# Optimization experiments

Hardware: AMD Instinct MI355X
Metric: run time of the kernel (lower is better)

## Reference

```python
import jax, jax.numpy as jnp
import numpy as np
from jax import lax

B, C, H, Wd = 8, 3, 256, 256
K = 32           # kernels
LAT = K * 8      # 256, latent dim
P = 7            # patch size
HALF = P // 2
S = 1024         # samples per image
PD = C * P * P   # 147
NEG = 0.01       # LeakyReLU slope
EPS = 1e-5


def setup_inputs() -> dict:
    key = jax.random.key(0)
    ks = jax.random.split(key, 20)
    x = jax.random.normal(ks[0], (B, C, H, Wd), dtype=jnp.float32)
    # patch centers must satisfy HALF <= c <= H-1-HALF (here [3, 252])
    anchors_hw = jax.random.randint(ks[1], (B, S, 2), HALF, H - HALF, dtype=jnp.int32)
    positives_hw = jax.random.randint(ks[2], (B, S, 2), HALF, H - HALF, dtype=jnp.int32)
    def w(k, shape, fan_in):
        return jax.random.normal(k, shape, dtype=jnp.float32) * (1.0 / np.sqrt(fan_in))
    inp = dict(x=x, anchors_hw=anchors_hw, positives_hw=positives_hw,
               w1=w(ks[3], (K, C, 3, 3), C * 9),        g1=jnp.ones((K,), jnp.float32),        b1=jnp.zeros((K,), jnp.float32),
               w2=w(ks[4], (2 * K, K, 3, 3), K * 9),    g2=jnp.ones((2 * K,), jnp.float32),    b2=jnp.zeros((2 * K,), jnp.float32),
               w3=w(ks[5], (4 * K, 2 * K, 3, 3), 2 * K * 9), g3=jnp.ones((4 * K,), jnp.float32), b3=jnp.zeros((4 * K,), jnp.float32),
               w4=w(ks[6], (8 * K, 4 * K, 3, 3), 4 * K * 9), g4=jnp.ones((8 * K,), jnp.float32), b4=jnp.zeros((8 * K,), jnp.float32),
               lin1_w=w(ks[7], (PD, LAT), LAT), lin1_b=jnp.zeros((PD,), jnp.float32),
               lin2_w=w(ks[8], (PD, PD), PD),   lin2_b=jnp.zeros((PD,), jnp.float32))
    return inp


def _conv(x, w):
    return lax.conv_general_dilated(x, w, (1, 1), 'SAME',
                                    dimension_numbers=('NCHW', 'OIHW', 'NCHW'))


def _bn(x, g, b):
    # training-mode BatchNorm2d: batch stats over (N,H,W)
    m = x.mean(axis=(0, 2, 3), keepdims=True)
    v = x.var(axis=(0, 2, 3), keepdims=True)
    return g[None, :, None, None] * (x - m) * lax.rsqrt(v + EPS) + b[None, :, None, None]


def _lrelu(x):
    return jnp.where(x >= 0, x, NEG * x)


def _forward(x, anchors_hw, positives_hw, w1, g1, b1, w2, g2, b2, w3, g3, b3,
             w4, g4, b4, lin1_w, lin1_b, lin2_w, lin2_b):
    feat = _lrelu(_bn(_conv(x, w1), g1, b1))
    feat = _lrelu(_bn(_conv(feat, w2), g2, b2))
    feat = _lrelu(_bn(_conv(feat, w3), g3, b3))
    feat = _lrelu(_bn(_conv(feat, w4), g4, b4))  # [B, LAT, H, W]

    fhwc = jnp.transpose(feat, (0, 2, 3, 1))  # [B,H,W,LAT]
    gather_pts = jax.vmap(lambda f, hw: f[hw[:, 0], hw[:, 1]])  # per-batch fancy gather
    W_anchors = gather_pts(fhwc, anchors_hw)      # [B,S,LAT]
    W_positives = gather_pts(fhwc, positives_hw)  # [B,S,LAT]

    def slice_one(img, hw):  # img [C,H,W], hw [2]
        return lax.dynamic_slice(img, (0, hw[0] - HALF, hw[1] - HALF), (C, P, P))
    patch_real = jax.vmap(jax.vmap(slice_one, in_axes=(None, 0)))(x, anchors_hw)  # [B,S,C,P,P]

    h = _lrelu(jnp.einsum('bsl,pl->bsp', W_anchors, lin1_w) + lin1_b)
    patch_recon = (jnp.einsum('bsp,qp->bsq', h, lin2_w) + lin2_b).reshape(x.shape[0], -1, C, P, P)
    return (feat, patch_real, patch_recon, W_anchors, W_positives)


def reference(x, anchors_hw, positives_hw, w1, g1, b1, w2, g2, b2, w3, g3, b3,
              w4, g4, b4, lin1_w, lin1_b, lin2_w, lin2_b):
    return _forward(x, anchors_hw, positives_hw, w1, g1, b1, w2, g2, b2,
                    w3, g3, b3, w4, g4, b4, lin1_w, lin1_b, lin2_w, lin2_b)
```

## Files before the change

kernel.cpp:

```cpp
#include <hip/hip_runtime.h>
#include <hip/hip_bf16.h>

typedef unsigned short u16;
typedef short bf16x8 __attribute__((ext_vector_type(8)));
typedef float f32x4 __attribute__((ext_vector_type(4)));
typedef unsigned short u16x8 __attribute__((ext_vector_type(8)));

#define PD 147

static const long OFF_PREAL = 134217728L;
static const long OFF_PRECON= 135421952L;
static const long OFF_WA    = 136626176L;
static const long OFF_WP    = 138723328L;

static const long RAW_SPLIT = 100663296L;

__device__ __forceinline__ float lrelu(float v){ return v >= 0.f ? v : 0.01f*v; }

__device__ __forceinline__ float bf2f(u16 u){
    union { unsigned int i; float f; } x; x.i = ((unsigned int)u) << 16; return x.f;
}
__device__ __forceinline__ u16 f2bf(float f){
    __hip_bfloat16 h = __float2bfloat16(f);
    return *reinterpret_cast<u16*>(&h);
}

__device__ __forceinline__ void gload16(const void* g, void* l){
    __builtin_amdgcn_global_load_lds((const __attribute__((address_space(1))) void*)g,
                                     (__attribute__((address_space(3))) void*)l, 16, 0, 0);
}

template<int CIN, int KOUT, bool SPLIT>
__global__ __launch_bounds__(512)
void conv_mfma(const u16* __restrict__ fin, const u16* __restrict__ wt,
               const float* __restrict__ ssin,
               void* __restrict__ out_, u16* __restrict__ rawhi,
               float* __restrict__ part)
{
    constexpr int CC = CIN / 32;
    constexpr int NS3 = CC * 3;
    constexpr int NF = KOUT / 64;
    constexpr int ABYTES = 2 * 324 * 32 * 2;
    constexpr int BQ = 3 * KOUT * 4;
    constexpr int NB3 = (BQ + 511) / 512;
    constexpr int BBYTES = 2 * BQ * 16;
    constexpr int EPIB = 256 * KOUT * 2;
    constexpr int SB = (ABYTES + BBYTES) > EPIB ? (ABYTES + BBYTES) : EPIB;
    __shared__ __align__(16) char smem[SB];
    u16* As = (u16*)smem;
    u16* Bs = (u16*)(smem + ABYTES);

    const int tid = threadIdx.x;
    const int w = tid >> 6, lane = tid & 63;
    const int wm = w >> 2, wn = w & 3;
    const int tile = blockIdx.x;
    const int tx0 = (tile & 15) << 4, ty0 = (tile >> 4) << 4;
    const int b = blockIdx.y;
    const long pixbase = (long)b << 16;
    const int hi = lane >> 4;
    const int quarter = lane & 3;

    f32x4 acc[8][NF];
#pragma unroll
    for (int m = 0; m < 8; m++)
#pragma unroll
        for (int n = 0; n < NF; n++) acc[m][n] = (f32x4){0.f,0.f,0.f,0.f};

    float sc8[8], sh8[8];
    auto load_ss = [&](int cc){
        int c0 = cc*32 + quarter*8;
#pragma unroll
        for (int j = 0; j < 8; j++){
            sc8[j] = ssin[c0 + j];
            sh8[j] = ssin[CIN + c0 + j];
        }
    };

    auto stage_a_round = [&](int cc, int buf, int r){
        int q = r*512 + w*64 + lane;
        int pf = q >> 2;
        int ly = pf / 18, lx = pf - ly*18;
        int gy = ty0 + ly - 1, gx = tx0 + lx - 1;
        bool ok = (q < 1296) && ((unsigned)gy < 256u) && ((unsigned)gx < 256u);
        u16x8 o = (u16x8){0,0,0,0,0,0,0,0};
        if (ok){
            u16x8 v = *(const u16x8*)(fin + ((pixbase + (gy<<8) + gx) * CIN + cc*32 + quarter*8));
#pragma unroll
            for (int j = 0; j < 8; j++)
                o[j] = f2bf(lrelu(sc8[j]*bf2f(v[j]) + sh8[j]));
        }
        if (q < 1296)
            *(u16x8*)(As + buf*(324*32) + q*8) = o;
    };
    auto stage_b3 = [&](int s, int buf){
        int cc = s / 3, dyr = s - cc*3;
        int t0 = dyr * 3;
        u16* dstbase = Bs + buf * (BQ*16/2);
#pragma unroll
        for (int r = 0; r < NB3; ++r){
            int q = r*512 + w*64 + lane;
            int tl = q / (KOUT*4);
            int qq = q - tl*(KOUT*4);
            int k = qq >> 2, bq = qq & 3;
            const u16* src = wt + (((long)(t0+tl)*KOUT + k) * CIN + cc*32 + bq*8);
            u16* dst = dstbase + (r*512 + w*64) * 8;
            if (q < BQ) gload16(src, dst);
        }
    };

    load_ss(0);
    stage_a_round(0, 0, 0); stage_a_round(0, 0, 1); stage_a_round(0, 0, 2);
    stage_b3(0, 0);
    __syncthreads();

#pragma unroll 1
    for (int s = 0; s < NS3; ++s){
        int cc = s / 3, dyr = s - cc*3;
        if (s + 1 < NS3) stage_b3(s + 1, (s + 1) & 1);
        if (cc + 1 < CC){
            if (dyr == 0) load_ss(cc + 1);
            stage_a_round(cc + 1, (cc + 1) & 1, dyr);
        }

        const u16* Ab = As + (cc & 1) * (324*32);
        const u16* Bb = Bs + (s & 1) * (BQ*16/2);
#pragma unroll
        for (int t = 0; t < 3; ++t){
            bf16x8 av[8];
#pragma unroll
            for (int m = 0; m < 8; m++){
                int pf = (wm*8 + m + dyr)*18 + (lane & 15) + t;
                av[m] = *(const bf16x8*)(Ab + pf*32 + hi*8);
            }
            bf16x8 bv[NF];
#pragma unroll
            for (int n = 0; n < NF; n++){
                int ch = (wn*NF + n)*16 + (lane & 15);
                bv[n] = *(const bf16x8*)(Bb + (t*KOUT + ch)*32 + hi*8);
            }
#pragma unroll
            for (int m = 0; m < 8; m++)
#pragma unroll
                for (int n = 0; n < NF; n++)
                    acc[m][n] = __builtin_amdgcn_mfma_f32_16x16x32_bf16(av[m], bv[n], acc[m][n], 0, 0, 0);
        }
        __syncthreads();
    }

    {
        const int bid = blockIdx.y * 256 + blockIdx.x;
        const long slot = (long)bid * 2 + wm;
#pragma unroll
        for (int n = 0; n < NF; n++){
            float s = 0.f, s2 = 0.f;
#pragma unroll
            for (int m = 0; m < 8; m++)
#pragma unroll
                for (int j = 0; j < 4; j++){
                    float v = acc[m][n][j];
                    s += v; s2 += v*v;
                }
            s += __shfl_down(s, 32); s2 += __shfl_down(s2, 32);
            s += __shfl_down(s, 16); s2 += __shfl_down(s2, 16);
            if (lane < 16){
                int ch = (wn*NF + n)*16 + lane;
                long off = (slot*KOUT + ch)*2;
                part[off]   = s;
                part[off+1] = s2;
            }
        }
    }

    {
        u16* ep = (u16*)smem;
        u16* outh = (u16*)out_;
        if (SPLIT && b >= 6) outh = rawhi - RAW_SPLIT;
#pragma unroll
        for (int m = 0; m < 8; m++)
#pragma unroll
            for (int n = 0; n < NF; n++){
                int ch = (wn*NF + n)*16 + (lane&15);
#pragma unroll
                for (int j = 0; j < 4; j++){
                    int px = wm*128 + m*16 + (lane>>4)*4 + j;
                    ep[px*KOUT + ch] = f2bf(acc[m][n][j]);
                }
            }
        __syncthreads();
        const int n16 = 256*KOUT/8;
        const int upr = KOUT*2;
        for (int i = tid; i < n16; i += 512){
            int py = i / upr;
            int rem = i - py*upr;
            long ga = (pixbase + ((ty0+py)<<8) + tx0) * KOUT + (long)rem*8;
            *(int4*)(outh + ga) = *(int4*)(ep + (long)i*8);
        }
    }
}

__global__ __launch_bounds__(256)
void conv1_direct(const float* __restrict__ x, const float* __restrict__ w1, u16* __restrict__ f1)
{
    __shared__ float wl[864];
    const int t = threadIdx.x;
    for (int i = t; i < 864; i += 256) wl[i] = w1[i];
    __syncthreads();
    const int y = blockIdx.x, b = blockIdx.y;
    float acc[32];
#pragma unroll
    for (int k = 0; k < 32; k++) acc[k] = 0.f;
    const long ib = (long)b*3*65536;
    for (int c = 0; c < 3; c++){
#pragma unroll
        for (int dy = 0; dy < 3; dy++){
            int gy = y + dy - 1;
#pragma unroll
            for (int dx = 0; dx < 3; dx++){
                int gx = t + dx - 1;
                float v = 0.f;
                if ((unsigned)gy < 256u && (unsigned)gx < 256u)
                    v = x[ib + c*65536 + (gy<<8) + gx];
                const float* wp = &wl[c*9 + dy*3 + dx];
#pragma unroll
                for (int k = 0; k < 32; k++) acc[k] += v * wp[k*27];
            }
        }
    }
    u16 ub[32];
#pragma unroll
    for (int k = 0; k < 32; k++) ub[k] = f2bf(acc[k]);
    u16* dst = f1 + ((long)(b*65536 + (y<<8) + t)) * 32;
#pragma unroll
    for (int j = 0; j < 4; j++) *(int4*)(dst + j*8) = *(int4*)(ub + j*8);
}

__global__ __launch_bounds__(256)
void prep_w(const float* __restrict__ w, u16* __restrict__ wt, int K, int C)
{
    int i = blockIdx.x*256 + threadIdx.x;
    if (i >= 9*K*C) return;
    int c = i % C; int r = i / C; int k = r % K; int tap = r / K;
    wt[i] = f2bf(w[((long)k*C + c)*9 + tap]);
}

template<int C>
__global__ __launch_bounds__(256)
void bn_stats_nhwc(const u16* __restrict__ f, float* __restrict__ part)
{
    constexpr int CQ = C/4;
    constexpr int SUBS = 256/CQ;
    const int t = threadIdx.x;
    const int cq = t & (CQ-1);
    const int sub = t / CQ;
    const long rowbase = (long)blockIdx.x * 512;
    float s[4] = {0,0,0,0}, q2[4] = {0,0,0,0};
    for (int r = sub; r < 512; r += SUBS){
        ushort4 v = *(const ushort4*)(f + (rowbase + r)*C + cq*4);
        float x0 = bf2f(v.x), x1 = bf2f(v.y), x2 = bf2f(v.z), x3 = bf2f(v.w);
        s[0]+=x0; q2[0]+=x0*x0; s[1]+=x1; q2[1]+=x1*x1;
        s[2]+=x2; q2[2]+=x2*x2; s[3]+=x3; q2[3]+=x3*x3;
    }
    __shared__ float r0[256], r1[256];
    for (int j = 0; j < 4; j++){
        r0[t] = s[j]; r1[t] = q2[j];
        __syncthreads();
        for (int st = 128; st >= CQ; st >>= 1){
            if (t < st){ r0[t] += r0[t+st]; r1[t] += r1[t+st]; }
            __syncthreads();
        }
        if (t < CQ){
            part[((long)blockIdx.x * C + t*4 + j)*2]     = r0[t];
            part[((long)blockIdx.x * C + t*4 + j)*2 + 1] = r1[t];
        }
        __syncthreads();
    }
}

__global__ __launch_bounds__(256)
void bn_stats_final2(const float* __restrict__ part, const float* __restrict__ g,
                     const float* __restrict__ bb, int C, int NB2, float* __restrict__ ss)
{
    const int c = blockIdx.x, t = threadIdx.x;
    float s = 0.f, s2 = 0.f;
    for (int i = t; i < NB2; i += 256){
        s  += part[((long)i*C + c)*2];
        s2 += part[((long)i*C + c)*2 + 1];
    }
    __shared__ float r0[256], r1[256];
    r0[t] = s; r1[t] = s2;
    __syncthreads();
    for (int st = 128; st > 0; st >>= 1){
        if (t < st){ r0[t] += r0[t+st]; r1[t] += r1[t+st]; }
        __syncthreads();
    }
    if (t == 0){
        const float invN = 1.f/524288.f;
        float m = r0[0]*invN;
        float v = r1[0]*invN - m*m;
        float sc = g[c]/sqrtf(v + 1e-5f);
        ss[c] = sc; ss[C+c] = bb[c] - m*sc;
    }
}

__global__ __launch_bounds__(256)
void bn_expand_t(const u16* __restrict__ rawlo, const u16* __restrict__ rawhi,
                 const float* __restrict__ ss, float* __restrict__ feat, int b0)
{
    __shared__ u16 lds[64*258];
    const int bid = blockIdx.x;
    const int b = b0 + (bid >> 10);
    const int px0 = (bid & 1023) * 64;
    const long p0 = (((long)(b<<16) + px0)) << 8;
    const u16* src = (b < 6) ? (rawlo + p0) : (rawhi + (p0 - RAW_SPLIT));
    const int t = threadIdx.x;
#pragma unroll
    for (int it = 0; it < 8; ++it){
        int i = it*256 + t;
        int px = i >> 5, u = i & 31;
        *(u16x8*)&lds[px*258 + u*8] = *(const u16x8*)(src + (long)i*8);
    }
    __syncthreads();
#pragma unroll
    for (int it = 0; it < 16; ++it){
        int idx = it*256 + t;
        int ch = idx >> 4;
        int q  = idx & 15;
        const float sc = ss[ch], sh = ss[256 + ch];
        float4 o;
        o.x = lrelu(sc*bf2f(lds[(q*4+0)*258 + ch]) + sh);
        o.y = lrelu(sc*bf2f(lds[(q*4+1)*258 + ch]) + sh);
        o.z = lrelu(sc*bf2f(lds[(q*4+2)*258 + ch]) + sh);
        o.w = lrelu(sc*bf2f(lds[(q*4+3)*258 + ch]) + sh);
        *(float4*)(feat + (((long)(b*256 + ch)) << 16) + px0 + q*4) = o;
    }
}

__global__ __launch_bounds__(256)
void gather_w_raw(const u16* __restrict__ rawlo, const u16* __restrict__ rawhi,
                  const float* __restrict__ ss, const int* __restrict__ hw,
                  float* __restrict__ outW)
{
    const int site = blockIdx.x;
    const int b = site >> 10;
    const int y = hw[site*2], x = hw[site*2 + 1];
    const int c = threadIdx.x;
    const long p = ((long)((b<<16) + (y<<8) + x)) << 8;
    const u16* base = (b < 6) ? (rawlo + p) : (rawhi + (p - RAW_SPLIT));
    float v = bf2f(base[c]);
    outW[(long)site*256 + c] = lrelu(ss[c]*v + ss[256 + c]);
}

__global__ __launch_bounds__(256)
void gather_patch(const float* __restrict__ x, const int* __restrict__ hw,
                  float* __restrict__ out)
{
    const long i = (long)blockIdx.x*256 + threadIdx.x;
    if (i >= 1204224L) return;
    const int px = (int)(i % 7);
    long r = i / 7;
    const int py = (int)(r % 7); r /= 7;
    const int c  = (int)(r % 3); r /= 3;
    const int s  = (int)(r % 1024);
    const int b  = (int)(r / 1024);
    const int site = b*1024 + s;
    const int yy = hw[site*2]     - 3 + py;
    const int xx = hw[site*2 + 1] - 3 + px;
    out[i] = x[(((long)(b*3 + c)) << 16) + ((long)yy << 8) + xx];
}

__global__ __launch_bounds__(256)
void mlp8(const float* __restrict__ Wa, const float* __restrict__ l1w,
          const float* __restrict__ l1b, const float* __restrict__ l2w,
          const float* __restrict__ l2b, float* __restrict__ out)
{
    __shared__ float wa[2048];
    __shared__ float h[8][152];
    const int blk = blockIdx.x;
    const int t = threadIdx.x;
#pragma unroll
    for (int it = 0; it < 8; ++it)
        wa[it*256 + t] = Wa[(long)blk*2048 + it*256 + t];
    __syncthreads();
    if (t < PD){
        float a[8] = {0,0,0,0,0,0,0,0};
        const float* wr = l1w + t*256;
#pragma unroll 4
        for (int l = 0; l < 256; ++l){
            float wv = wr[l];
#pragma unroll
            for (int g = 0; g < 8; ++g) a[g] += wa[g*256 + l]*wv;
        }
        float bb = l1b[t];
#pragma unroll
        for (int g = 0; g < 8; ++g) h[g][t] = lrelu(a[g] + bb);
    }
    __syncthreads();
    if (t < PD){
        float r[8] = {0,0,0,0,0,0,0,0};
        const float* wr = l2w + t*PD;
        for (int p = 0; p < PD; ++p){
            float wv = wr[p];
#pragma unroll
            for (int g = 0; g < 8; ++g) r[g] += h[g][p]*wv;
        }
        float bb = l2b[t];
#pragma unroll
        for (int g = 0; g < 8; ++g)
            out[((long)(blk*8 + g))*PD + t] = r[g] + bb;
    }
}

extern "C" void kernel_launch(void* const* d_in, const int* in_sizes, int n_in,
                              void* d_out, int out_size, void* d_ws, size_t ws_size,
                              hipStream_t stream)
{
    const float* x   = (const float*)d_in[0];
    const int*   anc = (const int*)  d_in[1];
    const int*   pos = (const int*)  d_in[2];
    const float* w1  = (const float*)d_in[3];
    const float* g1  = (const float*)d_in[4];
    const float* b1  = (const float*)d_in[5];
    const float* w2  = (const float*)d_in[6];
    const float* g2  = (const float*)d_in[7];
    const float* b2  = (const float*)d_in[8];
    const float* w3  = (const float*)d_in[9];
    const float* g3  = (const float*)d_in[10];
    const float* b3  = (const float*)d_in[11];
    const float* w4  = (const float*)d_in[12];
    const float* g4  = (const float*)d_in[13];
    const float* b4  = (const float*)d_in[14];
    const float* l1w = (const float*)d_in[15];
    const float* l1b = (const float*)d_in[16];
    const float* l2w = (const float*)d_in[17];
    const float* l2b = (const float*)d_in[18];

    float* feat = (float*)d_out;
    float* oPR  = feat + OFF_PREAL;
    float* oRC  = feat + OFF_PRECON;
    float* oWA  = feat + OFF_WA;
    float* oWP  = feat + OFF_WP;

    char* wsb = (char*)d_ws;
    u16* f2b = (u16*)wsb;
    u16* f3b = (u16*)(wsb + 67108864L);
    u16* f1b = (u16*)(wsb + 134217728L);

    u16* rawlo = (u16*)d_out + 167772160L;
    u16* rawhi = f2b;

    u16* Wt2 = (u16*)oWA;
    u16* Wt3 = Wt2 + 18432;
    u16* Wt4 = Wt3 + 73728;
    float* part = oWP;
    float* ss1 = oRC, *ss2 = oRC + 64, *ss3 = oRC + 192, *ss4 = oRC + 448;

    prep_w<<<72,   256, 0, stream>>>(w2, Wt2, 64, 32);
    prep_w<<<288,  256, 0, stream>>>(w3, Wt3, 128, 64);
    prep_w<<<1152, 256, 0, stream>>>(w4, Wt4, 256, 128);

    conv1_direct<<<dim3(256,8), 256, 0, stream>>>(x, w1, f1b);
    bn_stats_nhwc<32><<<1024, 256, 0, stream>>>(f1b, part);
    bn_stats_final2<<<32, 256, 0, stream>>>(part, g1, b1, 32, 1024, ss1);

    conv_mfma<32,64,false><<<dim3(256,8), 512, 0, stream>>>(f1b, Wt2, ss1, f2b, nullptr, part);
    bn_stats_final2<<<64, 256, 0, stream>>>(part, g2, b2, 64, 4096, ss2);

    conv_mfma<64,128,false><<<dim3(256,8), 512, 0, stream>>>(f2b, Wt3, ss2, f3b, nullptr, part);
    bn_stats_final2<<<128, 256, 0, stream>>>(part, g3, b3, 128, 4096, ss3);

    conv_mfma<128,256,true><<<dim3(256,8), 512, 0, stream>>>(f3b, Wt4, ss3, rawlo, rawhi, part);
    bn_stats_final2<<<256, 256, 0, stream>>>(part, g4, b4, 256, 4096, ss4);

    gather_w_raw<<<8192, 256, 0, stream>>>(rawlo, rawhi, ss4, anc, oWA);
    gather_w_raw<<<8192, 256, 0, stream>>>(rawlo, rawhi, ss4, pos, oWP);
    gather_patch<<<4704, 256, 0, stream>>>(x, anc, oPR);

    bn_expand_t<<<5120, 256, 0, stream>>>(rawlo, rawhi, ss4, feat, 0);
    bn_expand_t<<<1024, 256, 0, stream>>>(rawlo, rawhi, ss4, feat, 5);
    bn_expand_t<<<2048, 256, 0, stream>>>(rawlo, rawhi, ss4, feat, 6);

    mlp8<<<1024, 256, 0, stream>>>(oWA, l1w, l1b, l2w, l2b, oRC);
}
```

Measured before the change: 803.3 us.

## Split conv output channels across blocks with smaller 256-thread tiles

Restructures the MFMA conv kernel so each 256-thread block computes a 16x16 pixel tile for only 64 output channels, with a grid dimension over channel groups. It stages per-tap weight slices instead of three taps per step and single-buffers the activation tile, which stalls on a barrier at each channel chunk. Per-block BN partials are reduced in shared memory before being written. The aim is lower register and LDS use so more blocks fit per CU, at the cost of recomputing the BN+LReLU input staging once per channel group and losing the overlap of activation loads with compute.

```diff
diff --git a/kernel.cpp b/kernel.cpp
--- a/kernel.cpp
+++ b/kernel.cpp
@@ -31,20 +31,17 @@
 }
 
 template<int CIN, int KOUT, bool SPLIT>
-__global__ __launch_bounds__(512)
+__global__ __launch_bounds__(256, 4)
 void conv_mfma(const u16* __restrict__ fin, const u16* __restrict__ wt,
                const float* __restrict__ ssin,
                void* __restrict__ out_, u16* __restrict__ rawhi,
                float* __restrict__ part)
 {
     constexpr int CC = CIN / 32;
-    constexpr int NS3 = CC * 3;
-    constexpr int NF = KOUT / 64;
-    constexpr int ABYTES = 2 * 324 * 32 * 2;
-    constexpr int BQ = 3 * KOUT * 4;
-    constexpr int NB3 = (BQ + 511) / 512;
-    constexpr int BBYTES = 2 * BQ * 16;
-    constexpr int EPIB = 256 * KOUT * 2;
+    constexpr int NSTEPS = CC * 9;
+    constexpr int ABYTES = 324 * 32 * 2;
+    constexpr int BBYTES = 2 * 64 * 32 * 2;
+    constexpr int EPIB = 256 * 64 * 2;
     constexpr int SB = (ABYTES + BBYTES) > EPIB ? (ABYTES + BBYTES) : EPIB;
     __shared__ __align__(16) char smem[SB];
     u16* As = (u16*)smem;
@@ -52,109 +49,96 @@
 
     const int tid = threadIdx.x;
     const int w = tid >> 6, lane = tid & 63;
-    const int wm = w >> 2, wn = w & 3;
     const int tile = blockIdx.x;
     const int tx0 = (tile & 15) << 4, ty0 = (tile >> 4) << 4;
-    const int b = blockIdx.y;
+    const int bz = blockIdx.y;
+    const int b  = blockIdx.z;
     const long pixbase = (long)b << 16;
     const int hi = lane >> 4;
-    const int quarter = lane & 3;
-
-    f32x4 acc[8][NF];
-#pragma unroll
-    for (int m = 0; m < 8; m++)
-#pragma unroll
-        for (int n = 0; n < NF; n++) acc[m][n] = (f32x4){0.f,0.f,0.f,0.f};
-
-    float sc8[8], sh8[8];
-    auto load_ss = [&](int cc){
+    const int quarter = tid & 3;
+
+    f32x4 acc[4][4];
+#pragma unroll
+    for (int m = 0; m < 4; m++)
+#pragma unroll
+        for (int n = 0; n < 4; n++) acc[m][n] = (f32x4){0.f,0.f,0.f,0.f};
+
+    auto stage_a = [&](int cc){
+        float sc8[8], sh8[8];
         int c0 = cc*32 + quarter*8;
 #pragma unroll
         for (int j = 0; j < 8; j++){
             sc8[j] = ssin[c0 + j];
             sh8[j] = ssin[CIN + c0 + j];
         }
+#pragma unroll
+        for (int r = 0; r < 6; ++r){
+            int q = r*256 + tid;
+            if (q < 1296){
+                int pf = q >> 2;
+                int ly = pf / 18, lx = pf - ly*18;
+                int gy = ty0 + ly - 1, gx = tx0 + lx - 1;
+                u16x8 o = (u16x8){0,0,0,0,0,0,0,0};
+                if ((unsigned)gy < 256u && (unsigned)gx < 256u){
+                    u16x8 v = *(const u16x8*)(fin + ((pixbase + (gy<<8) + gx) * CIN + cc*32 + quarter*8));
+#pragma unroll
+                    for (int j = 0; j < 8; j++)
+                        o[j] = f2bf(lrelu(sc8[j]*bf2f(v[j]) + sh8[j]));
+                }
+                *(u16x8*)(As + q*8) = o;
+            }
+        }
     };
-
-    auto stage_a_round = [&](int cc, int buf, int r){
-        int q = r*512 + w*64 + lane;
-        int pf = q >> 2;
-        int ly = pf / 18, lx = pf - ly*18;
-        int gy = ty0 + ly - 1, gx = tx0 + lx - 1;
-        bool ok = (q < 1296) && ((unsigned)gy < 256u) && ((unsigned)gx < 256u);
-        u16x8 o = (u16x8){0,0,0,0,0,0,0,0};
-        if (ok){
-            u16x8 v = *(const u16x8*)(fin + ((pixbase + (gy<<8) + gx) * CIN + cc*32 + quarter*8));
-#pragma unroll
-            for (int j = 0; j < 8; j++)
-                o[j] = f2bf(lrelu(sc8[j]*bf2f(v[j]) + sh8[j]));
-        }
-        if (q < 1296)
-            *(u16x8*)(As + buf*(324*32) + q*8) = o;
+    auto stage_b = [&](int s, int buf){
+        int cc2 = s / 9, tap = s - cc2*9;
+        const u16* src = wt + (((long)tap*KOUT + bz*64 + (tid>>2)) * CIN + cc2*32 + (tid&3)*8);
+        u16* dst = Bs + buf*2048 + (w*64)*8;
+        gload16(src, dst);
     };
-    auto stage_b3 = [&](int s, int buf){
-        int cc = s / 3, dyr = s - cc*3;
-        int t0 = dyr * 3;
-        u16* dstbase = Bs + buf * (BQ*16/2);
-#pragma unroll
-        for (int r = 0; r < NB3; ++r){
-            int q = r*512 + w*64 + lane;
-            int tl = q / (KOUT*4);
-            int qq = q - tl*(KOUT*4);
-            int k = qq >> 2, bq = qq & 3;
-            const u16* src = wt + (((long)(t0+tl)*KOUT + k) * CIN + cc*32 + bq*8);
-            u16* dst = dstbase + (r*512 + w*64) * 8;
-            if (q < BQ) gload16(src, dst);
-        }
-    };
-
-    load_ss(0);
-    stage_a_round(0, 0, 0); stage_a_round(0, 0, 1); stage_a_round(0, 0, 2);
-    stage_b3(0, 0);
+
+    stage_a(0);
+    stage_b(0, 0);
     __syncthreads();
 
 #pragma unroll 1
-    for (int s = 0; s < NS3; ++s){
-        int cc = s / 3, dyr = s - cc*3;
-        if (s + 1 < NS3) stage_b3(s + 1, (s + 1) & 1);
-        if (cc + 1 < CC){
-            if (dyr == 0) load_ss(cc + 1);
-            stage_a_round(cc + 1, (cc + 1) & 1, dyr);
-        }
-
-        const u16* Ab = As + (cc & 1) * (324*32);
-        const u16* Bb = Bs + (s & 1) * (BQ*16/2);
-#pragma unroll
-        for (int t = 0; t < 3; ++t){
-            bf16x8 av[8];
-#pragma unroll
-            for (int m = 0; m < 8; m++){
-                int pf = (wm*8 + m + dyr)*18 + (lane & 15) + t;
-                av[m] = *(const bf16x8*)(Ab + pf*32 + hi*8);
-            }
-            bf16x8 bv[NF];
-#pragma unroll
-            for (int n = 0; n < NF; n++){
-                int ch = (wn*NF + n)*16 + (lane & 15);
-                bv[n] = *(const bf16x8*)(Bb + (t*KOUT + ch)*32 + hi*8);
-            }
-#pragma unroll
-            for (int m = 0; m < 8; m++)
-#pragma unroll
-                for (int n = 0; n < NF; n++)
-                    acc[m][n] = __builtin_amdgcn_mfma_f32_16x16x32_bf16(av[m], bv[n], acc[m][n], 0, 0, 0);
-        }
-        __syncthreads();
+    for (int s = 0; s < NSTEPS; ++s){
+        int cc = s / 9, tap = s - cc*9;
+        if (s + 1 < NSTEPS) stage_b(s + 1, (s + 1) & 1);
+
+        int dy = tap / 3, dx = tap - dy*3;
+        const u16* Bb = Bs + (s & 1) * 2048;
+        bf16x8 av[4];
+#pragma unroll
+        for (int m = 0; m < 4; m++){
+            int pf = (w*4 + m + dy)*18 + (lane & 15) + dx;
+            av[m] = *(const bf16x8*)(As + pf*32 + hi*8);
+        }
+        bf16x8 bv[4];
+#pragma unroll
+        for (int n = 0; n < 4; n++){
+            int chl = n*16 + (lane & 15);
+            bv[n] = *(const bf16x8*)(Bb + chl*32 + hi*8);
+        }
+#pragma unroll
+        for (int m = 0; m < 4; m++)
+#pragma unroll
+            for (int n = 0; n < 4; n++)
+                acc[m][n] = __builtin_amdgcn_mfma_f32_16x16x32_bf16(av[m], bv[n], acc[m][n], 0, 0, 0);
+
+        __syncthreads();
+        if (tap == 8 && cc + 1 < CC){
+            stage_a(cc + 1);
+            __syncthreads();
+        }
     }
 
     {
-        const int bid = blockIdx.y * 256 + blockIdx.x;
-        const long slot = (long)bid * 2 + wm;
-#pragma unroll
-        for (int n = 0; n < NF; n++){
+        float* sred = (float*)smem;
+#pragma unroll
+        for (int n = 0; n < 4; n++){
             float s = 0.f, s2 = 0.f;
 #pragma unroll
-            for (int m = 0; m < 8; m++)
+            for (int m = 0; m < 4; m++)
 #pragma unroll
                 for (int j = 0; j < 4; j++){
                     float v = acc[m][n][j];
@@ -163,36 +147,49 @@
             s += __shfl_down(s, 32); s2 += __shfl_down(s2, 32);
             s += __shfl_down(s, 16); s2 += __shfl_down(s2, 16);
             if (lane < 16){
-                int ch = (wn*NF + n)*16 + lane;
-                long off = (slot*KOUT + ch)*2;
-                part[off]   = s;
-                part[off+1] = s2;
+                int ch = n*16 + lane;
+                sred[w*64 + ch]       = s;
+                sred[256 + w*64 + ch] = s2;
             }
         }
+        __syncthreads();
+        if (tid < 64){
+            float S = 0.f, S2 = 0.f;
+#pragma unroll
+            for (int w2 = 0; w2 < 4; w2++){
+                S  += sred[w2*64 + tid];
+                S2 += sred[256 + w2*64 + tid];
+            }
+            long i = (long)b*256 + tile;
+            long off = (i*KOUT + bz*64 + tid)*2;
+            part[off]   = S;
+            part[off+1] = S2;
+        }
+        __syncthreads();
     }
 
     {
         u16* ep = (u16*)smem;
+#pragma unroll
+        for (int m = 0; m < 4; m++)
+#pragma unroll
+            for (int n = 0; n < 4; n++){
+                int ch = n*16 + (lane & 15);
+#pragma unroll
+                for (int j = 0; j < 4; j++){
+                    int px = (w*4 + m)*16 + (lane>>4)*4 + j;
+                    ep[px*64 + ch] = f2bf(acc[m][n][j]);
+                }
+            }
+        __syncthreads();
         u16* outh = (u16*)out_;
         if (SPLIT && b >= 6) outh = rawhi - RAW_SPLIT;
 #pragma unroll
-        for (int m = 0; m < 8; m++)
-#pragma unroll
-            for (int n = 0; n < NF; n++){
-                int ch = (wn*NF + n)*16 + (lane&15);
-#pragma unroll
-                for (int j = 0; j < 4; j++){
-                    int px = wm*128 + m*16 + (lane>>4)*4 + j;
-                    ep[px*KOUT + ch] = f2bf(acc[m][n][j]);
-                }
-            }
-        __syncthreads();
-        const int n16 = 256*KOUT/8;
-        const int upr = KOUT*2;
-        for (int i = tid; i < n16; i += 512){
-            int py = i / upr;
-            int rem = i - py*upr;
-            long ga = (pixbase + ((ty0+py)<<8) + tx0) * KOUT + (long)rem*8;
+        for (int it = 0; it < 8; ++it){
+            int i = it*256 + tid;
+            int px = i >> 3, u = i & 7;
+            int py = px >> 4, pxc = px & 15;
+            long ga = (pixbase + ((ty0+py)<<8) + tx0 + pxc) * KOUT + bz*64 + (long)u*8;
             *(int4*)(outh + ga) = *(int4*)(ep + (long)i*8);
         }
     }
@@ -462,14 +459,14 @@
     bn_stats_nhwc<32><<<1024, 256, 0, stream>>>(f1b, part);
     bn_stats_final2<<<32, 256, 0, stream>>>(part, g1, b1, 32, 1024, ss1);
 
-    conv_mfma<32,64,false><<<dim3(256,8), 512, 0, stream>>>(f1b, Wt2, ss1, f2b, nullptr, part);
-    bn_stats_final2<<<64, 256, 0, stream>>>(part, g2, b2, 64, 4096, ss2);
-
-    conv_mfma<64,128,false><<<dim3(256,8), 512, 0, stream>>>(f2b, Wt3, ss2, f3b, nullptr, part);
-    bn_stats_final2<<<128, 256, 0, stream>>>(part, g3, b3, 128, 4096, ss3);
-
-    conv_mfma<128,256,true><<<dim3(256,8), 512, 0, stream>>>(f3b, Wt4, ss3, rawlo, rawhi, part);
-    bn_stats_final2<<<256, 256, 0, stream>>>(part, g4, b4, 256, 4096, ss4);
+    conv_mfma<32,64,false><<<dim3(256,1,8), 256, 0, stream>>>(f1b, Wt2, ss1, f2b, nullptr, part);
+    bn_stats_final2<<<64, 256, 0, stream>>>(part, g2, b2, 64, 2048, ss2);
+
+    conv_mfma<64,128,false><<<dim3(256,2,8), 256, 0, stream>>>(f2b, Wt3, ss2, f3b, nullptr, part);
+    bn_stats_final2<<<128, 256, 0, stream>>>(part, g3, b3, 128, 2048, ss3);
+
+    conv_mfma<128,256,true><<<dim3(256,4,8), 256, 0, stream>>>(f3b, Wt4, ss3, rawlo, rawhi, part);
+    bn_stats_final2<<<256, 256, 0, stream>>>(part, g4, b4, 256, 2048, ss4);
 
     gather_w_raw<<<8192, 256, 0, stream>>>(rawlo, rawhi, ss4, anc, oWA);
     gather_w_raw<<<8192, 256, 0, stream>>>(rawlo, rawhi, ss4, pos, oWP);
```

Result: faster. 766.5 us (-4.6%).
